# Optimization experiments

Measured on AMD Instinct MI355X. Metric: run time of the kernel, lower is better.

## Reference

```python
import jax, jax.numpy as jnp
import numpy as np

EMB = 1024
HEADS = 16
DEPTH = EMB // HEADS
B, S = 8, 1024


def setup_inputs() -> dict:
    key = jax.random.key(0)
    ks = jax.random.split(key, 12)
    sc = 0.02
    return {
        "q": jax.random.normal(ks[0], (B, S, EMB), jnp.float32),
        "k": jax.random.normal(ks[1], (B, S, EMB), jnp.float32),
        "v": jax.random.normal(ks[2], (B, S, EMB), jnp.float32),
        # per-head Dense weights stacked: [H, EMB, DEPTH], biases [H, DEPTH]
        "Wq": jax.random.normal(ks[3], (HEADS, EMB, DEPTH), jnp.float32) * sc,
        "bq": jnp.zeros((HEADS, DEPTH), jnp.float32),
        "Wk": jax.random.normal(ks[4], (HEADS, EMB, DEPTH), jnp.float32) * sc,
        "bk": jnp.zeros((HEADS, DEPTH), jnp.float32),
        "Wv": jax.random.normal(ks[5], (HEADS, EMB, DEPTH), jnp.float32) * sc,
        "bv": jnp.zeros((HEADS, DEPTH), jnp.float32),
        # output Dense: [EMB, EMB], bias [EMB]
        "Wo": jax.random.normal(ks[6], (EMB, EMB), jnp.float32) * sc,
        "bo": jnp.zeros((EMB,), jnp.float32),
    }


def reference(q, k, v, Wq, bq, Wk, bk, Wv, bv, Wo, bo):
    # Per-head Dense projections, batched over heads via einsum.
    # qh: [B, H, S, DEPTH]
    qh = jnp.einsum("bsd,hde->bhse", q, Wq) + bq[None, :, None, :]
    kh = jnp.einsum("bsd,hde->bhse", k, Wk) + bk[None, :, None, :]
    vh = jnp.einsum("bsd,hde->bhse", v, Wv) + bv[None, :, None, :]
    # Scaled dot-product attention per head: logits [B, H, Sq, Sk]
    scale = 1.0 / jnp.sqrt(jnp.asarray(DEPTH, jnp.float32))
    logits = jnp.einsum("bhqe,bhke->bhqk", qh, kh) * scale
    attn = jax.nn.softmax(logits, axis=-1)
    ctx = jnp.einsum("bhqk,bhke->bhqe", attn, vh)  # [B, H, S, DEPTH]
    # concat heads along last axis (head order preserved)
    ctx = jnp.transpose(ctx, (0, 2, 1, 3)).reshape(B, S, EMB)
    return ctx @ Wo + bo
```

## Files before the change

### kernel.cpp

```cpp
#include <hip/hip_runtime.h>
#include <hip/hip_bf16.h>
#include <stdint.h>

typedef __bf16 bf16;
typedef __attribute__((ext_vector_type(8))) __bf16 bf16x8;
typedef __attribute__((ext_vector_type(4))) float f32x4;

#define GLD(g, l) __builtin_amdgcn_global_load_lds( \
    (const __attribute__((address_space(1))) void*)(g), \
    (__attribute__((address_space(3))) void*)(l), 16, 0, 0)

__device__ __forceinline__ f32x4 mfma16(bf16x8 a, bf16x8 b, f32x4 c) {
  return __builtin_amdgcn_mfma_f32_16x16x32_bf16(a, b, c, 0, 0, 0);
}

template <typename ST>
__global__ void transpose_k(const ST* __restrict__ src, bf16* __restrict__ dst,
                            int sld, int dld, int sdiv, int sA, int sB, int dA, int dB)
{
  __shared__ bf16 t[32][33];
  const int z = blockIdx.z;
  const ST* s = src + (size_t)(z / sdiv) * sA + (size_t)(z % sdiv) * sB;
  bf16* d = dst + (size_t)(z / sdiv) * dA + (size_t)(z % sdiv) * dB;
  const int c0 = blockIdx.x * 32, r0 = blockIdx.y * 32;
  const int tx = threadIdx.x, ty = threadIdx.y;
#pragma unroll
  for (int i = 0; i < 32; i += 8)
    t[ty + i][tx] = (bf16)(float)s[(r0 + ty + i) * sld + c0 + tx];
  __syncthreads();
#pragma unroll
  for (int i = 0; i < 32; i += 8)
    d[(c0 + ty + i) * dld + r0 + tx] = t[tx][ty + i];
}

__global__ __launch_bounds__(256) void proj_qkv(
    const float* __restrict__ Aq, const float* __restrict__ Ak,
    const float* __restrict__ Av, const bf16* __restrict__ WT,
    const float* __restrict__ bq, const float* __restrict__ bk,
    const float* __restrict__ bv, bf16* __restrict__ Cb,
    float cscale)
{
  __shared__ bf16 sA[128 * 72];
  __shared__ bf16 sB[128 * 64];
  const int tid = threadIdx.x;
  const int wave = tid >> 6, lane = tid & 63;
  const int lr = lane & 15, quad = lane >> 4, kq = quad * 8;
  const int n0 = blockIdx.y * 128;
  const int mseg = blockIdx.x * 128;
  const int seg = mseg >> 13;
  const int m0 = mseg & 8191;
  const int wr = (wave >> 1) * 64, wc = (wave & 1) * 64;

  const float* A = (seg == 0) ? Aq : (seg == 1) ? Ak : Av;
  const float* bias = (seg == 0) ? bq : (seg == 1) ? bk : bv;
  const float cmul = (seg == 0) ? cscale : 1.0f;
  const bf16* Bt = WT + (size_t)seg * (1 << 20);
  bf16* C = Cb + (size_t)seg * (8192 * 1024);

  f32x4 acc[4][4];
#pragma unroll
  for (int i = 0; i < 4; i++)
#pragma unroll
    for (int j = 0; j < 4; j++)
#pragma unroll
      for (int e = 0; e < 4; e++) acc[i][j][e] = 0.f;

  const int ar = tid >> 1, ach = (tid & 1) * 32;
  const float* aPtr = A + (size_t)(m0 + ar) * 1024 + ach;
  const int brow = tid >> 3;
  const int bc = ((tid & 7) ^ (brow & 7)) * 8;
  const bf16* bPtr = Bt + (size_t)(n0 + brow) * 1024 + bc;
  bf16* sBd = sB + tid * 8;

  for (int k0 = 0; k0 < 1024; k0 += 64) {
    GLD(bPtr + k0,             sBd);
    GLD(bPtr + 32 * 1024 + k0, sBd + 2048);
    GLD(bPtr + 64 * 1024 + k0, sBd + 4096);
    GLD(bPtr + 96 * 1024 + k0, sBd + 6144);
    float4 f[8];
#pragma unroll
    for (int j = 0; j < 8; j++) f[j] = *(const float4*)(aPtr + k0 + j * 4);
    __syncthreads();
#pragma unroll
    for (int j = 0; j < 4; j++) {
      bf16x8 p;
      p[0] = (bf16)f[2*j].x; p[1] = (bf16)f[2*j].y;
      p[2] = (bf16)f[2*j].z; p[3] = (bf16)f[2*j].w;
      p[4] = (bf16)f[2*j+1].x; p[5] = (bf16)f[2*j+1].y;
      p[6] = (bf16)f[2*j+1].z; p[7] = (bf16)f[2*j+1].w;
      *(bf16x8*)(sA + ar * 72 + ach + j * 8) = p;
    }
    __syncthreads();
#pragma unroll
    for (int kk = 0; kk < 64; kk += 32) {
      bf16x8 af[4], bfr[4];
#pragma unroll
      for (int i = 0; i < 4; i++)
        af[i] = *(const bf16x8*)(sA + (wr + i * 16 + lr) * 72 + kk + kq);
#pragma unroll
      for (int i = 0; i < 4; i++) {
        const int pos = (((kk >> 3) + quad) ^ (lr & 7)) * 8;
        bfr[i] = *(const bf16x8*)(sB + (wc + i * 16 + lr) * 64 + pos);
      }
#pragma unroll
      for (int im = 0; im < 4; im++)
#pragma unroll
        for (int in = 0; in < 4; in++)
          acc[im][in] = mfma16(af[im], bfr[in], acc[im][in]);
    }
  }
  __syncthreads();

  const int qd = quad * 4;
  float bv4[4];
#pragma unroll
  for (int in = 0; in < 4; in++) bv4[in] = bias[n0 + wc + in * 16 + lr];
#pragma unroll
  for (int im = 0; im < 4; im++) {
    const int row = m0 + wr + im * 16 + qd;
#pragma unroll
    for (int in = 0; in < 4; in++) {
      const int col = n0 + wc + in * 16 + lr;
#pragma unroll
      for (int i = 0; i < 4; i++)
        C[(size_t)(row + i) * 1024 + col] = (bf16)((acc[im][in][i] + bv4[in]) * cmul);
    }
  }
}

__global__ __launch_bounds__(256) void gemm_a16_c32(
    const bf16* __restrict__ A, const bf16* __restrict__ Bt,
    const float* __restrict__ bias, float* __restrict__ C)
{
  __shared__ bf16 sA[128 * 64];
  __shared__ bf16 sB[128 * 64];
  const int tid = threadIdx.x;
  const int wave = tid >> 6, lane = tid & 63;
  const int lr = lane & 15, quad = lane >> 4, kq = quad * 8;
  const int m0 = blockIdx.x * 128, n0 = blockIdx.y * 128;
  const int wr = (wave >> 1) * 64, wc = (wave & 1) * 64;

  f32x4 acc[4][4];
#pragma unroll
  for (int i = 0; i < 4; i++)
#pragma unroll
    for (int j = 0; j < 4; j++)
#pragma unroll
      for (int e = 0; e < 4; e++) acc[i][j][e] = 0.f;

  const int srow = tid >> 3;
  const int sc = ((tid & 7) ^ (srow & 7)) * 8;
  const bf16* aPtr = A + (size_t)(m0 + srow) * 1024 + sc;
  const bf16* bPtr = Bt + (size_t)(n0 + srow) * 1024 + sc;
  bf16* sAd = sA + tid * 8;
  bf16* sBd = sB + tid * 8;

  for (int k0 = 0; k0 < 1024; k0 += 64) {
    GLD(aPtr + k0,             sAd);
    GLD(aPtr + 32 * 1024 + k0, sAd + 2048);
    GLD(aPtr + 64 * 1024 + k0, sAd + 4096);
    GLD(aPtr + 96 * 1024 + k0, sAd + 6144);
    GLD(bPtr + k0,             sBd);
    GLD(bPtr + 32 * 1024 + k0, sBd + 2048);
    GLD(bPtr + 64 * 1024 + k0, sBd + 4096);
    GLD(bPtr + 96 * 1024 + k0, sBd + 6144);
    __syncthreads();
#pragma unroll
    for (int kk = 0; kk < 64; kk += 32) {
      bf16x8 af[4], bfr[4];
#pragma unroll
      for (int i = 0; i < 4; i++) {
        const int pos = (((kk >> 3) + quad) ^ (lr & 7)) * 8;
        af[i]  = *(const bf16x8*)(sA + (wr + i * 16 + lr) * 64 + pos);
        bfr[i] = *(const bf16x8*)(sB + (wc + i * 16 + lr) * 64 + pos);
      }
#pragma unroll
      for (int im = 0; im < 4; im++)
#pragma unroll
        for (int in = 0; in < 4; in++)
          acc[im][in] = mfma16(af[im], bfr[in], acc[im][in]);
    }
    __syncthreads();
  }

  const int qd = quad * 4;
  float bv4[4];
#pragma unroll
  for (int in = 0; in < 4; in++) bv4[in] = bias[n0 + wc + in * 16 + lr];
#pragma unroll
  for (int im = 0; im < 4; im++) {
    const int row = m0 + wr + im * 16 + qd;
#pragma unroll
    for (int in = 0; in < 4; in++) {
      const int col = n0 + wc + in * 16 + lr;
#pragma unroll
      for (int i = 0; i < 4; i++)
        C[(size_t)(row + i) * 1024 + col] = acc[im][in][i] + bv4[in];
    }
  }
}

__global__ __launch_bounds__(256) void attn_k(
    const bf16* __restrict__ Q, const bf16* __restrict__ Kh,
    const bf16* __restrict__ Vt, bf16* __restrict__ O)
{
  __shared__ bf16 sK[64 * 72];
  __shared__ bf16 sV[64 * 72];
  __shared__ bf16 sP[128 * 72];
  const int h = blockIdx.x, b = blockIdx.y, q0 = blockIdx.z * 128;
  const int tid = threadIdx.x, wave = tid >> 6, lane = tid & 63;
  const int lr = lane & 15, quad = lane >> 4, kq = quad * 8;
  const int wq = wave * 32;

  const bf16* Qb = Q + (size_t)(b * 1024 + q0) * 1024 + h * 64;
  const bf16* Kb = Kh + (size_t)(b * 1024) * 1024 + h * 64;
  const bf16* Vb = Vt + (size_t)(b * 16 + h) * 65536;

  bf16x8 qf[2][2];
#pragma unroll
  for (int rg = 0; rg < 2; rg++)
#pragma unroll
    for (int ks = 0; ks < 2; ks++)
      qf[rg][ks] = *(const bf16x8*)(Qb + (wq + rg * 16 + lr) * 1024 + ks * 32 + kq);

  f32x4 o[2][4];
  float rsum[2][4];
#pragma unroll
  for (int rg = 0; rg < 2; rg++) {
#pragma unroll
    for (int et = 0; et < 4; et++)
#pragma unroll
      for (int e = 0; e < 4; e++) o[rg][et][e] = 0.f;
#pragma unroll
    for (int i = 0; i < 4; i++) rsum[rg][i] = 0.f;
  }

  const int r = tid >> 3;
  const int c = (tid & 7) * 8;

  for (int kv0 = 0; kv0 < 1024; kv0 += 64) {
    bf16x8 k1 = *(const bf16x8*)(Kb + (size_t)(kv0 + r) * 1024 + c);
    bf16x8 k2 = *(const bf16x8*)(Kb + (size_t)(kv0 + 32 + r) * 1024 + c);
    bf16x8 v1 = *(const bf16x8*)(Vb + (size_t)r * 1024 + kv0 + c);
    bf16x8 v2 = *(const bf16x8*)(Vb + (size_t)(32 + r) * 1024 + kv0 + c);
    __syncthreads();
    *(bf16x8*)(sK + r * 72 + c) = k1;
    *(bf16x8*)(sK + (32 + r) * 72 + c) = k2;
    *(bf16x8*)(sV + r * 72 + c) = v1;
    *(bf16x8*)(sV + (32 + r) * 72 + c) = v2;
    __syncthreads();

    f32x4 sc[2][4];
#pragma unroll
    for (int nt = 0; nt < 4; nt++) {
      bf16x8 kf0 = *(const bf16x8*)(sK + (nt * 16 + lr) * 72 + kq);
      bf16x8 kf1 = *(const bf16x8*)(sK + (nt * 16 + lr) * 72 + 32 + kq);
#pragma unroll
      for (int rg = 0; rg < 2; rg++) {
        f32x4 z;
#pragma unroll
        for (int e = 0; e < 4; e++) z[e] = 0.f;
        z = mfma16(qf[rg][0], kf0, z);
        z = mfma16(qf[rg][1], kf1, z);
        sc[rg][nt] = z;
      }
    }

#pragma unroll
    for (int rg = 0; rg < 2; rg++)
#pragma unroll
      for (int i = 0; i < 4; i++) {
        float p0 = exp2f(sc[rg][0][i]);
        float p1 = exp2f(sc[rg][1][i]);
        float p2 = exp2f(sc[rg][2][i]);
        float p3 = exp2f(sc[rg][3][i]);
        rsum[rg][i] += (p0 + p1) + (p2 + p3);
        const int prow = (wq + rg * 16 + quad * 4 + i) * 72;
        sP[prow + 0 * 16 + lr] = (bf16)p0;
        sP[prow + 1 * 16 + lr] = (bf16)p1;
        sP[prow + 2 * 16 + lr] = (bf16)p2;
        sP[prow + 3 * 16 + lr] = (bf16)p3;
      }
    __syncthreads();

#pragma unroll
    for (int et = 0; et < 4; et++) {
      bf16x8 vf0 = *(const bf16x8*)(sV + (et * 16 + lr) * 72 + kq);
      bf16x8 vf1 = *(const bf16x8*)(sV + (et * 16 + lr) * 72 + 32 + kq);
#pragma unroll
      for (int rg = 0; rg < 2; rg++) {
        bf16x8 pa = *(const bf16x8*)(sP + (wq + rg * 16 + lr) * 72 + kq);
        bf16x8 pb = *(const bf16x8*)(sP + (wq + rg * 16 + lr) * 72 + 32 + kq);
        o[rg][et] = mfma16(pa, vf0, o[rg][et]);
        o[rg][et] = mfma16(pb, vf1, o[rg][et]);
      }
    }
  }

#pragma unroll
  for (int rg = 0; rg < 2; rg++)
#pragma unroll
    for (int i = 0; i < 4; i++) {
      float rs = rsum[rg][i];
#pragma unroll
      for (int off = 1; off < 16; off <<= 1)
        rs += __shfl_xor(rs, off, 64);
      rsum[rg][i] = 1.f / rs;
    }

  bf16* Ob = O + (size_t)(b * 1024 + q0) * 1024 + h * 64;
#pragma unroll
  for (int rg = 0; rg < 2; rg++)
#pragma unroll
    for (int i = 0; i < 4; i++) {
      const int row = wq + rg * 16 + quad * 4 + i;
#pragma unroll
      for (int et = 0; et < 4; et++)
        Ob[row * 1024 + et * 16 + lr] = (bf16)(o[rg][et][i] * rsum[rg][i]);
    }
}

extern "C" void kernel_launch(void* const* d_in, const int* in_sizes, int n_in,
                              void* d_out, int out_size, void* d_ws, size_t ws_size,
                              hipStream_t stream)
{
  const float* q  = (const float*)d_in[0];
  const float* k  = (const float*)d_in[1];
  const float* v  = (const float*)d_in[2];
  const float* Wq = (const float*)d_in[3];
  const float* bq = (const float*)d_in[4];
  const float* Wk = (const float*)d_in[5];
  const float* bk = (const float*)d_in[6];
  const float* Wv = (const float*)d_in[7];
  const float* bv = (const float*)d_in[8];
  const float* Wo = (const float*)d_in[9];
  const float* bo = (const float*)d_in[10];
  float* out = (float*)d_out;
  bf16* ws = (bf16*)d_ws;

  const int MB = 1 << 20;
  bf16* WT  = ws;
  bf16* WoT = ws + 3 * MB;
  bf16* qkv = ws + 4 * MB;
  bf16* qh  = qkv;
  bf16* kh  = qkv + 8 * MB;
  bf16* vh  = qkv + 16 * MB;
  bf16* vt  = (bf16*)d_out;
  bf16* ctx = vh;

  const float cscale = 0.1803368801111601f;

  dim3 tb(32, 8);
  transpose_k<float><<<dim3(2, 32, 16), tb, 0, stream>>>(Wq, WT,          64, 1024, 16, 0, 65536, 0, 65536);
  transpose_k<float><<<dim3(2, 32, 16), tb, 0, stream>>>(Wk, WT + 1 * MB, 64, 1024, 16, 0, 65536, 0, 65536);
  transpose_k<float><<<dim3(2, 32, 16), tb, 0, stream>>>(Wv, WT + 2 * MB, 64, 1024, 16, 0, 65536, 0, 65536);
  transpose_k<float><<<dim3(32, 32, 1), tb, 0, stream>>>(Wo, WoT, 1024, 1024, 1, 0, 0, 0, 0);

  proj_qkv<<<dim3(192, 8), 256, 0, stream>>>(q, k, v, WT, bq, bk, bv, qkv, cscale);

  transpose_k<bf16><<<dim3(2, 32, 128), tb, 0, stream>>>(vh, vt, 1024, 1024, 16,
                                                         1048576, 64, 1048576, 65536);

  attn_k<<<dim3(16, 8, 8), 256, 0, stream>>>(qh, kh, vt, ctx);

  gemm_a16_c32<<<dim3(64, 8), 256, 0, stream>>>(ctx, WoT, bo, out);
}
```

Before: 374.5 us.

## Pre-cast q/k to bf16, fuse V transpose into projection epilogue, merge weight transposes

The q and k activations are now cast to bf16 in a separate vectorised kernel, so the projection GEMM can stage its A tiles with async global-to-LDS loads and an XOR swizzle. The v path still converts fp32 on the fly, but its epilogue writes V directly in transposed per-head layout, which removes the separate V transpose kernel. The Q/K/V weight transposes are merged into one launch, and attention now writes its context in place over qh. The intent is to cut a kernel launch and a round trip of V through memory, and to speed up A staging, at the cost of an extra full read and write of q and k for the cast.

Result: faster. 362.9 us (-3.1%).

```diff
diff --git a/kernel.cpp b/kernel.cpp
--- a/kernel.cpp
+++ b/kernel.cpp
@@ -4,6 +4,7 @@
 
 typedef __bf16 bf16;
 typedef __attribute__((ext_vector_type(8))) __bf16 bf16x8;
+typedef __attribute__((ext_vector_type(4))) __bf16 bf16x4;
 typedef __attribute__((ext_vector_type(4))) float f32x4;
 
 #define GLD(g, l) __builtin_amdgcn_global_load_lds( \
@@ -14,33 +15,65 @@
   return __builtin_amdgcn_mfma_f32_16x16x32_bf16(a, b, c, 0, 0, 0);
 }
 
-template <typename ST>
-__global__ void transpose_k(const ST* __restrict__ src, bf16* __restrict__ dst,
-                            int sld, int dld, int sdiv, int sA, int sB, int dA, int dB)
+__global__ void wtrans3(const float* __restrict__ Wq, const float* __restrict__ Wk,
+                        const float* __restrict__ Wv, bf16* __restrict__ WT)
 {
   __shared__ bf16 t[32][33];
-  const int z = blockIdx.z;
-  const ST* s = src + (size_t)(z / sdiv) * sA + (size_t)(z % sdiv) * sB;
-  bf16* d = dst + (size_t)(z / sdiv) * dA + (size_t)(z % sdiv) * dB;
+  const int w = blockIdx.z;
+  const float* W = (w == 0) ? Wq : (w == 1) ? Wk : Wv;
+  const int h = blockIdx.x >> 1;
+  const int c0 = (blockIdx.x & 1) * 32;
+  const int r0 = blockIdx.y * 32;
+  const float* s = W + (size_t)h * 65536;
+  bf16* d = WT + (size_t)w * (1 << 20) + (size_t)h * 65536;
+  const int tx = threadIdx.x, ty = threadIdx.y;
+#pragma unroll
+  for (int i = 0; i < 32; i += 8)
+    t[ty + i][tx] = (bf16)s[(r0 + ty + i) * 64 + c0 + tx];
+  __syncthreads();
+#pragma unroll
+  for (int i = 0; i < 32; i += 8)
+    d[(c0 + ty + i) * 1024 + r0 + tx] = t[tx][ty + i];
+}
+
+__global__ void wtransO(const float* __restrict__ src, bf16* __restrict__ dst)
+{
+  __shared__ bf16 t[32][33];
   const int c0 = blockIdx.x * 32, r0 = blockIdx.y * 32;
   const int tx = threadIdx.x, ty = threadIdx.y;
 #pragma unroll
   for (int i = 0; i < 32; i += 8)
-    t[ty + i][tx] = (bf16)(float)s[(r0 + ty + i) * sld + c0 + tx];
+    t[ty + i][tx] = (bf16)src[(r0 + ty + i) * 1024 + c0 + tx];
   __syncthreads();
 #pragma unroll
   for (int i = 0; i < 32; i += 8)
-    d[(c0 + ty + i) * dld + r0 + tx] = t[tx][ty + i];
+    dst[(c0 + ty + i) * 1024 + r0 + tx] = t[tx][ty + i];
+}
+
+__global__ __launch_bounds__(256) void cast2(const float* __restrict__ q,
+                                             const float* __restrict__ k,
+                                             bf16* __restrict__ qc,
+                                             bf16* __restrict__ kc)
+{
+  const float* s = blockIdx.y ? k : q;
+  bf16* d = blockIdx.y ? kc : qc;
+  const size_t i = ((size_t)blockIdx.x * 256 + threadIdx.x) * 8;
+  float4 a = *(const float4*)(s + i);
+  float4 b = *(const float4*)(s + i + 4);
+  bf16x8 p;
+  p[0] = (bf16)a.x; p[1] = (bf16)a.y; p[2] = (bf16)a.z; p[3] = (bf16)a.w;
+  p[4] = (bf16)b.x; p[5] = (bf16)b.y; p[6] = (bf16)b.z; p[7] = (bf16)b.w;
+  *(bf16x8*)(d + i) = p;
 }
 
 __global__ __launch_bounds__(256) void proj_qkv(
-    const float* __restrict__ Aq, const float* __restrict__ Ak,
-    const float* __restrict__ Av, const bf16* __restrict__ WT,
+    const bf16* __restrict__ qc, const bf16* __restrict__ kc,
+    const float* __restrict__ v, const bf16* __restrict__ WT,
     const float* __restrict__ bq, const float* __restrict__ bk,
-    const float* __restrict__ bv, bf16* __restrict__ Cb,
-    float cscale)
-{
-  __shared__ bf16 sA[128 * 72];
+    const float* __restrict__ bv, bf16* __restrict__ qh,
+    bf16* __restrict__ kh, bf16* __restrict__ vt, float cscale)
+{
+  __shared__ bf16 sA[128 * 64];
   __shared__ bf16 sB[128 * 64];
   const int tid = threadIdx.x;
   const int wave = tid >> 6, lane = tid & 63;
@@ -51,11 +84,8 @@
   const int m0 = mseg & 8191;
   const int wr = (wave >> 1) * 64, wc = (wave & 1) * 64;
 
-  const float* A = (seg == 0) ? Aq : (seg == 1) ? Ak : Av;
   const float* bias = (seg == 0) ? bq : (seg == 1) ? bk : bv;
-  const float cmul = (seg == 0) ? cscale : 1.0f;
   const bf16* Bt = WT + (size_t)seg * (1 << 20);
-  bf16* C = Cb + (size_t)seg * (8192 * 1024);
 
   f32x4 acc[4][4];
 #pragma unroll
@@ -65,65 +95,116 @@
 #pragma unroll
       for (int e = 0; e < 4; e++) acc[i][j][e] = 0.f;
 
-  const int ar = tid >> 1, ach = (tid & 1) * 32;
-  const float* aPtr = A + (size_t)(m0 + ar) * 1024 + ach;
-  const int brow = tid >> 3;
-  const int bc = ((tid & 7) ^ (brow & 7)) * 8;
-  const bf16* bPtr = Bt + (size_t)(n0 + brow) * 1024 + bc;
+  const int srow = tid >> 3;
+  const int scol = ((tid & 7) ^ (srow & 7)) * 8;
+  const bf16* bPtr = Bt + (size_t)(n0 + srow) * 1024 + scol;
   bf16* sBd = sB + tid * 8;
-
-  for (int k0 = 0; k0 < 1024; k0 += 64) {
-    GLD(bPtr + k0,             sBd);
-    GLD(bPtr + 32 * 1024 + k0, sBd + 2048);
-    GLD(bPtr + 64 * 1024 + k0, sBd + 4096);
-    GLD(bPtr + 96 * 1024 + k0, sBd + 6144);
-    float4 f[8];
-#pragma unroll
-    for (int j = 0; j < 8; j++) f[j] = *(const float4*)(aPtr + k0 + j * 4);
-    __syncthreads();
-#pragma unroll
-    for (int j = 0; j < 4; j++) {
-      bf16x8 p;
-      p[0] = (bf16)f[2*j].x; p[1] = (bf16)f[2*j].y;
-      p[2] = (bf16)f[2*j].z; p[3] = (bf16)f[2*j].w;
-      p[4] = (bf16)f[2*j+1].x; p[5] = (bf16)f[2*j+1].y;
-      p[6] = (bf16)f[2*j+1].z; p[7] = (bf16)f[2*j+1].w;
-      *(bf16x8*)(sA + ar * 72 + ach + j * 8) = p;
-    }
-    __syncthreads();
-#pragma unroll
-    for (int kk = 0; kk < 64; kk += 32) {
-      bf16x8 af[4], bfr[4];
-#pragma unroll
-      for (int i = 0; i < 4; i++)
-        af[i] = *(const bf16x8*)(sA + (wr + i * 16 + lr) * 72 + kk + kq);
-#pragma unroll
-      for (int i = 0; i < 4; i++) {
-        const int pos = (((kk >> 3) + quad) ^ (lr & 7)) * 8;
-        bfr[i] = *(const bf16x8*)(sB + (wc + i * 16 + lr) * 64 + pos);
-      }
-#pragma unroll
-      for (int im = 0; im < 4; im++)
-#pragma unroll
-        for (int in = 0; in < 4; in++)
-          acc[im][in] = mfma16(af[im], bfr[in], acc[im][in]);
-    }
-  }
-  __syncthreads();
+  bf16* sAd = sA + tid * 8;
+  const bf16* Ab = (seg == 1) ? kc : qc;
+  const bf16* aPtr = Ab + (size_t)(m0 + srow) * 1024 + scol;
+  const int ar = tid >> 1, ach2 = tid & 1;
+  const float* vPtr = v + (size_t)(m0 + ar) * 1024 + ach2 * 32;
+
+  if (seg < 2) {
+    for (int k0 = 0; k0 < 1024; k0 += 64) {
+      GLD(aPtr + k0,             sAd);
+      GLD(aPtr + 32 * 1024 + k0, sAd + 2048);
+      GLD(aPtr + 64 * 1024 + k0, sAd + 4096);
+      GLD(aPtr + 96 * 1024 + k0, sAd + 6144);
+      GLD(bPtr + k0,             sBd);
+      GLD(bPtr + 32 * 1024 + k0, sBd + 2048);
+      GLD(bPtr + 64 * 1024 + k0, sBd + 4096);
+      GLD(bPtr + 96 * 1024 + k0, sBd + 6144);
+      __syncthreads();
+#pragma unroll
+      for (int kk = 0; kk < 64; kk += 32) {
+        bf16x8 af[4], bfr[4];
+#pragma unroll
+        for (int i = 0; i < 4; i++) {
+          const int pos = (((kk >> 3) + quad) ^ (lr & 7)) * 8;
+          af[i]  = *(const bf16x8*)(sA + (wr + i * 16 + lr) * 64 + pos);
+          bfr[i] = *(const bf16x8*)(sB + (wc + i * 16 + lr) * 64 + pos);
+        }
+#pragma unroll
+        for (int im = 0; im < 4; im++)
+#pragma unroll
+          for (int in = 0; in < 4; in++)
+            acc[im][in] = mfma16(af[im], bfr[in], acc[im][in]);
+      }
+      __syncthreads();
+    }
+  } else {
+    for (int k0 = 0; k0 < 1024; k0 += 64) {
+      float4 f[8];
+#pragma unroll
+      for (int j = 0; j < 8; j++) f[j] = *(const float4*)(vPtr + k0 + j * 4);
+      __syncthreads();
+      GLD(bPtr + k0,             sBd);
+      GLD(bPtr + 32 * 1024 + k0, sBd + 2048);
+      GLD(bPtr + 64 * 1024 + k0, sBd + 4096);
+      GLD(bPtr + 96 * 1024 + k0, sBd + 6144);
+#pragma unroll
+      for (int j = 0; j < 4; j++) {
+        bf16x8 p;
+        p[0] = (bf16)f[2*j].x;   p[1] = (bf16)f[2*j].y;
+        p[2] = (bf16)f[2*j].z;   p[3] = (bf16)f[2*j].w;
+        p[4] = (bf16)f[2*j+1].x; p[5] = (bf16)f[2*j+1].y;
+        p[6] = (bf16)f[2*j+1].z; p[7] = (bf16)f[2*j+1].w;
+        const int cj = ach2 * 4 + j;
+        *(bf16x8*)(sA + ar * 64 + ((cj ^ (ar & 7)) * 8)) = p;
+      }
+      __syncthreads();
+#pragma unroll
+      for (int kk = 0; kk < 64; kk += 32) {
+        bf16x8 af[4], bfr[4];
+#pragma unroll
+        for (int i = 0; i < 4; i++) {
+          const int pos = (((kk >> 3) + quad) ^ (lr & 7)) * 8;
+          af[i]  = *(const bf16x8*)(sA + (wr + i * 16 + lr) * 64 + pos);
+          bfr[i] = *(const bf16x8*)(sB + (wc + i * 16 + lr) * 64 + pos);
+        }
+#pragma unroll
+        for (int im = 0; im < 4; im++)
+#pragma unroll
+          for (int in = 0; in < 4; in++)
+            acc[im][in] = mfma16(af[im], bfr[in], acc[im][in]);
+      }
+    }
+  }
 
   const int qd = quad * 4;
   float bv4[4];
 #pragma unroll
   for (int in = 0; in < 4; in++) bv4[in] = bias[n0 + wc + in * 16 + lr];
-#pragma unroll
-  for (int im = 0; im < 4; im++) {
-    const int row = m0 + wr + im * 16 + qd;
-#pragma unroll
-    for (int in = 0; in < 4; in++) {
-      const int col = n0 + wc + in * 16 + lr;
-#pragma unroll
-      for (int i = 0; i < 4; i++)
-        C[(size_t)(row + i) * 1024 + col] = (bf16)((acc[im][in][i] + bv4[in]) * cmul);
+
+  if (seg < 2) {
+    bf16* C = (seg == 0) ? qh : kh;
+    const float cmul = (seg == 0) ? cscale : 1.0f;
+#pragma unroll
+    for (int im = 0; im < 4; im++) {
+      const int row = m0 + wr + im * 16 + qd;
+#pragma unroll
+      for (int in = 0; in < 4; in++) {
+        const int col = n0 + wc + in * 16 + lr;
+#pragma unroll
+        for (int i = 0; i < 4; i++)
+          C[(size_t)(row + i) * 1024 + col] = (bf16)((acc[im][in][i] + bv4[in]) * cmul);
+      }
+    }
+  } else {
+#pragma unroll
+    for (int im = 0; im < 4; im++) {
+      const int row = m0 + wr + im * 16 + qd;
+      const int b = row >> 10, sin = row & 1023;
+#pragma unroll
+      for (int in = 0; in < 4; in++) {
+        const int col = n0 + wc + in * 16 + lr;
+        const int h = col >> 6, e = col & 63;
+        bf16x4 pk;
+#pragma unroll
+        for (int i = 0; i < 4; i++) pk[i] = (bf16)(acc[im][in][i] + bv4[in]);
+        *(bf16x4*)(vt + (size_t)(b * 16 + h) * 65536 + e * 1024 + sin) = pk;
+      }
     }
   }
 }
@@ -201,8 +282,8 @@
 }
 
 __global__ __launch_bounds__(256) void attn_k(
-    const bf16* __restrict__ Q, const bf16* __restrict__ Kh,
-    const bf16* __restrict__ Vt, bf16* __restrict__ O)
+    const bf16* Q, const bf16* __restrict__ Kh,
+    const bf16* __restrict__ Vt, bf16* O)
 {
   __shared__ bf16 sK[64 * 72];
   __shared__ bf16 sV[64 * 72];
@@ -340,28 +421,24 @@
 
   const int MB = 1 << 20;
   bf16* WT  = ws;
-  bf16* WoT = ws + 3 * MB;
-  bf16* qkv = ws + 4 * MB;
-  bf16* qh  = qkv;
-  bf16* kh  = qkv + 8 * MB;
-  bf16* vh  = qkv + 16 * MB;
-  bf16* vt  = (bf16*)d_out;
-  bf16* ctx = vh;
+  bf16* qh  = ws + 3 * MB;
+  bf16* kh  = ws + 11 * MB;
+  bf16* vt  = ws + 19 * MB;
+  bf16* WoT = ws + 27 * MB;
+  bf16* qc  = (bf16*)d_out;
+  bf16* kc  = (bf16*)d_out + 8 * MB;
 
   const float cscale = 0.1803368801111601f;
 
   dim3 tb(32, 8);
-  transpose_k<float><<<dim3(2, 32, 16), tb, 0, stream>>>(Wq, WT,          64, 1024, 16, 0, 65536, 0, 65536);
-  transpose_k<float><<<dim3(2, 32, 16), tb, 0, stream>>>(Wk, WT + 1 * MB, 64, 1024, 16, 0, 65536, 0, 65536);
-  transpose_k<float><<<dim3(2, 32, 16), tb, 0, stream>>>(Wv, WT + 2 * MB, 64, 1024, 16, 0, 65536, 0, 65536);
-  transpose_k<float><<<dim3(32, 32, 1), tb, 0, stream>>>(Wo, WoT, 1024, 1024, 1, 0, 0, 0, 0);
-
-  proj_qkv<<<dim3(192, 8), 256, 0, stream>>>(q, k, v, WT, bq, bk, bv, qkv, cscale);
-
-  transpose_k<bf16><<<dim3(2, 32, 128), tb, 0, stream>>>(vh, vt, 1024, 1024, 16,
-                                                         1048576, 64, 1048576, 65536);
-
-  attn_k<<<dim3(16, 8, 8), 256, 0, stream>>>(qh, kh, vt, ctx);
-
-  gemm_a16_c32<<<dim3(64, 8), 256, 0, stream>>>(ctx, WoT, bo, out);
-}
+  wtrans3<<<dim3(32, 32, 3), tb, 0, stream>>>(Wq, Wk, Wv, WT);
+  wtransO<<<dim3(32, 32), tb, 0, stream>>>(Wo, WoT);
+  cast2<<<dim3(4096, 2), 256, 0, stream>>>(q, k, qc, kc);
+
+  proj_qkv<<<dim3(192, 8), 256, 0, stream>>>(qc, kc, v, WT, bq, bk, bv,
+                                             qh, kh, vt, cscale);
+
+  attn_k<<<dim3(16, 8, 8), 256, 0, stream>>>(qh, kh, vt, qh);
+
+  gemm_a16_c32<<<dim3(64, 8), 256, 0, stream>>>(qh, WoT, bo, out);
+}
```
